# Optimization experiments

Measured on AMD Instinct MI355X. Metric: run time of the kernel, lower is better.

Reference implementation:

```python
import jax, jax.numpy as jnp
import numpy as np

S, B, E = 2048, 2, 768
H = 12
D = E // H  # 64
SCALE = D ** -0.5


def setup_inputs() -> dict:
    key = jax.random.key(0)
    ks = jax.random.split(key, 10)
    inp = {
        "query": jax.random.normal(ks[0], (S, B, E), dtype=jnp.float32),
        "attn_bias": jax.random.normal(ks[1], (B * H, S, S), dtype=jnp.float32) * 0.1,
        "key_padding_mask": jax.random.randint(ks[2], (B, S), 0, 2).astype(bool),
        "Wq": jax.random.normal(ks[3], (E, E), dtype=jnp.float32) * (E ** -0.5),
        "bq": jnp.zeros((E,), dtype=jnp.float32),
        "Wk": jax.random.normal(ks[4], (E, E), dtype=jnp.float32) * (E ** -0.5),
        "bk": jnp.zeros((E,), dtype=jnp.float32),
        "Wv": jax.random.normal(ks[5], (E, E), dtype=jnp.float32) * (E ** -0.5),
        "bv": jnp.zeros((E,), dtype=jnp.float32),
        "Wo": jax.random.normal(ks[6], (E, E), dtype=jnp.float32) * (E ** -0.5),
        "bo": jnp.zeros((E,), dtype=jnp.float32),
    }
    return inp


def reference(query, attn_bias, key_padding_mask, Wq, bq, Wk, bk, Wv, bv, Wo, bo):
    s, b, e = query.shape
    # projections (torch Linear: x @ W.T + b)
    q = (query @ Wq.T + bq) * SCALE
    k = query @ Wk.T + bk
    v = query @ Wv.T + bv
    # [s, b, e] -> [b*h, s, d]
    def to_heads(x):
        return x.reshape(s, b * H, D).transpose(1, 0, 2)
    q, k, v = to_heads(q), to_heads(k), to_heads(v)
    # scores [b*h, s_q, s_k]
    scores = jnp.einsum('nqd,nkd->nqk', q, k) + attn_bias
    # key padding mask: [b, s_k] -> broadcast over heads and queries
    scores = scores.reshape(b, H, s, s)
    scores = jnp.where(key_padding_mask[:, None, None, :], -jnp.inf, scores)
    scores = scores.reshape(b * H, s, s)
    probs = jax.nn.softmax(scores, axis=-1)
    attn = jnp.einsum('nqk,nkd->nqd', probs, v)  # [b*h, s, d]
    attn = attn.transpose(1, 0, 2).reshape(s, b, e)
    return attn @ Wo.T + bo
```

## Files before the change

kernel.cpp:

```cpp
#include <hip/hip_runtime.h>
#include <hip/hip_bf16.h>

typedef __attribute__((ext_vector_type(8))) short s16x8;
typedef __attribute__((ext_vector_type(4))) float f32x4;
typedef unsigned short u16;
typedef unsigned int u32;

#define SDIM 2048
#define BDIM 2
#define HDIM 12
#define DDIM 64
#define EDIM 768
#define MDIM 4096
#define SCALE_Q 0.125f
#define KSPLIT 1024
#define NIT (KSPLIT / 32)
#define HFRAG 131072

static __device__ __forceinline__ f32x4 zero4() {
    f32x4 v; v[0] = v[1] = v[2] = v[3] = 0.f; return v;
}

static __device__ __forceinline__ u16 f2b(float x) {
    u32 u = __builtin_bit_cast(u32, x);
    u32 lsb = (u >> 16) & 1u;
    u += 0x7fffu + lsb;
    return (u16)(u >> 16);
}

static __device__ __forceinline__ f32x4 mfma16(s16x8 a, s16x8 b, f32x4 c) {
    return __builtin_amdgcn_mfma_f32_16x16x32_bf16(a, b, c, 0, 0, 0);
}

static __device__ __forceinline__ void gload_lds16(const void* g, void* l) {
    __builtin_amdgcn_global_load_lds(
        (const __attribute__((address_space(1))) void*)g,
        (__attribute__((address_space(3))) void*)l, 16, 0, 0);
}

__global__ void mask_bits_kernel(const u32* __restrict__ raw, u32* __restrict__ outbits) {
    __shared__ int okInt, okFloat;
    int t = threadIdx.x;
    if (t == 0) { okInt = 1; okFloat = 1; }
    __syncthreads();
    int li = 1, lf = 1;
    for (int i = t; i < 1024; i += blockDim.x) {
        u32 v = raw[i];
        if (v > 1u) li = 0;
        if (v != 0u && v != 0x3F800000u) lf = 0;
    }
    if (!li) atomicAnd(&okInt, 0);
    if (!lf) atomicAnd(&okFloat, 0);
    __syncthreads();
    const unsigned char* rb = (const unsigned char*)raw;
    if (t < (BDIM * SDIM) / 32) {
        u32 bits = 0;
        for (int j = 0; j < 32; ++j) {
            int i = t * 32 + j;
            int v;
            if (okInt)        v = (int)raw[i];
            else if (okFloat) v = (raw[i] != 0u) ? 1 : 0;
            else              v = (int)rb[i];
            bits |= (v ? 1u : 0u) << j;
        }
        outbits[t] = bits;
    }
}

__global__ __launch_bounds__(256) void conv_f32_bf16(
    const float* __restrict__ s, u16* __restrict__ d, int n8)
{
    int i = blockIdx.x * 256 + threadIdx.x;
    if (i >= n8) return;
    float4 x0 = ((const float4*)s)[(size_t)i * 2];
    float4 x1 = ((const float4*)s)[(size_t)i * 2 + 1];
    uint4 o;
    o.x = (u32)f2b(x0.x) | ((u32)f2b(x0.y) << 16);
    o.y = (u32)f2b(x0.z) | ((u32)f2b(x0.w) << 16);
    o.z = (u32)f2b(x1.x) | ((u32)f2b(x1.y) << 16);
    o.w = (u32)f2b(x1.z) | ((u32)f2b(x1.w) << 16);
    ((uint4*)d)[i] = o;
}

__global__ __launch_bounds__(256) void gemm_qkv(
    const u16* __restrict__ A,
    const u16* __restrict__ wq, const u16* __restrict__ wk, const u16* __restrict__ wv,
    const float* __restrict__ bq, const float* __restrict__ bk, const float* __restrict__ bv,
    u16* __restrict__ qout, u16* __restrict__ kout, u16* __restrict__ vout)
{
    __shared__ u16 Al[4096];
    __shared__ u16 Bl[4096];
    int tid = threadIdx.x;
    int lane = tid & 63, w = tid >> 6;
    int r16 = lane & 15, g4 = lane >> 4;
    int wm = w >> 1, wn = w & 1;
    int mb = blockIdx.x * 64;
    int nbg = blockIdx.y * 64;
    int mid = nbg / EDIM;
    int nb = nbg - mid * EDIM;
    const u16* W = (mid == 0) ? wq : (mid == 1) ? wk : wv;
    const float* bias = (mid == 0) ? bq : (mid == 1) ? bk : bv;
    float scale = (mid == 0) ? SCALE_Q : 1.0f;

    f32x4 acc[2][2];
    acc[0][0] = zero4(); acc[0][1] = zero4(); acc[1][0] = zero4(); acc[1][1] = zero4();

    for (int kb = 0; kb < EDIM; kb += 64) {
        __syncthreads();
        #pragma unroll
        for (int j = 0; j < 2; ++j) {
            int c = w * 2 + j;
            gload_lds16(&A[(size_t)(mb + lane) * EDIM + kb + c * 8], (char*)Al + c * 1024);
            gload_lds16(&W[(size_t)(nb + lane) * EDIM + kb + c * 8], (char*)Bl + c * 1024);
        }
        asm volatile("s_waitcnt vmcnt(0)" ::: "memory");
        __syncthreads();
        #pragma unroll
        for (int kk = 0; kk < 2; ++kk) {
            s16x8 a[2], b[2];
            #pragma unroll
            for (int mi = 0; mi < 2; ++mi)
                a[mi] = *(const s16x8*)&Al[(kk * 4 + g4) * 512 + (wm * 32 + mi * 16 + r16) * 8];
            #pragma unroll
            for (int ni = 0; ni < 2; ++ni)
                b[ni] = *(const s16x8*)&Bl[(kk * 4 + g4) * 512 + (wn * 32 + ni * 16 + r16) * 8];
            #pragma unroll
            for (int mi = 0; mi < 2; ++mi)
                #pragma unroll
                for (int ni = 0; ni < 2; ++ni)
                    acc[mi][ni] = mfma16(a[mi], b[ni], acc[mi][ni]);
        }
    }

    #pragma unroll
    for (int mi = 0; mi < 2; ++mi) {
        #pragma unroll
        for (int ni = 0; ni < 2; ++ni) {
            int n = nb + wn * 32 + ni * 16 + r16;
            float bv_ = bias[n];
            #pragma unroll
            for (int r = 0; r < 4; ++r) {
                int m = mb + wm * 32 + mi * 16 + g4 * 4 + r;
                float c = (acc[mi][ni][r] + bv_) * scale;
                int s_ = m >> 1, b_ = m & 1, h_ = n >> 6, d_ = n & 63;
                if (mid == 0) {
                    qout[((size_t)(b_ * HDIM + h_) * SDIM + s_) * DDIM + d_] = f2b(c);
                } else if (mid == 1) {
                    size_t p = (size_t)(b_ * HDIM + h_) * HFRAG
                             + (size_t)(s_ >> 4) * 1024 + (size_t)((d_ >> 5) & 1) * 512
                             + (size_t)(((d_ >> 3) & 3) * 16 + (s_ & 15)) * 8 + (d_ & 7);
                    kout[p] = f2b(c);
                } else {
                    size_t p = (size_t)(b_ * HDIM + h_) * HFRAG
                             + (size_t)(s_ >> 5) * 2048 + (size_t)((d_ >> 4) & 3) * 512
                             + (size_t)(((s_ >> 3) & 3) * 16 + (d_ & 15)) * 8 + (s_ & 7);
                    vout[p] = f2b(c);
                }
            }
        }
    }
}

__global__ __launch_bounds__(256) void gemm_out(
    const u16* __restrict__ A, const u16* __restrict__ Wb,
    const float* __restrict__ bias, float* __restrict__ out_rm)
{
    __shared__ u16 Al[4096];
    __shared__ u16 Bl[4096];
    int tid = threadIdx.x;
    int lane = tid & 63, w = tid >> 6;
    int r16 = lane & 15, g4 = lane >> 4;
    int wm = w >> 1, wn = w & 1;
    int mb = blockIdx.x * 64, nb = blockIdx.y * 64;

    f32x4 acc[2][2];
    acc[0][0] = zero4(); acc[0][1] = zero4(); acc[1][0] = zero4(); acc[1][1] = zero4();

    for (int kb = 0; kb < EDIM; kb += 64) {
        __syncthreads();
        #pragma unroll
        for (int j = 0; j < 2; ++j) {
            int c = w * 2 + j;
            gload_lds16(&A[(size_t)(mb + lane) * EDIM + kb + c * 8], (char*)Al + c * 1024);
            gload_lds16(&Wb[(size_t)(nb + lane) * EDIM + kb + c * 8], (char*)Bl + c * 1024);
        }
        asm volatile("s_waitcnt vmcnt(0)" ::: "memory");
        __syncthreads();
        #pragma unroll
        for (int kk = 0; kk < 2; ++kk) {
            s16x8 a[2], b[2];
            #pragma unroll
            for (int mi = 0; mi < 2; ++mi)
                a[mi] = *(const s16x8*)&Al[(kk * 4 + g4) * 512 + (wm * 32 + mi * 16 + r16) * 8];
            #pragma unroll
            for (int ni = 0; ni < 2; ++ni)
                b[ni] = *(const s16x8*)&Bl[(kk * 4 + g4) * 512 + (wn * 32 + ni * 16 + r16) * 8];
            #pragma unroll
            for (int mi = 0; mi < 2; ++mi)
                #pragma unroll
                for (int ni = 0; ni < 2; ++ni)
                    acc[mi][ni] = mfma16(a[mi], b[ni], acc[mi][ni]);
        }
    }

    #pragma unroll
    for (int mi = 0; mi < 2; ++mi) {
        #pragma unroll
        for (int ni = 0; ni < 2; ++ni) {
            int n = nb + wn * 32 + ni * 16 + r16;
            float bv_ = bias[n];
            #pragma unroll
            for (int r = 0; r < 4; ++r) {
                int m = mb + wm * 32 + mi * 16 + g4 * 4 + r;
                out_rm[(size_t)m * EDIM + n] = acc[mi][ni][r] + bv_;
            }
        }
    }
}

struct KV { s16x8 k0, k1, k2, k3, v0, v1, v2, v3; };

__global__ __launch_bounds__(128) void attn_fused(
    const u16* __restrict__ qw, const u16* __restrict__ kf_g,
    const u16* __restrict__ vf_g, const float* __restrict__ bias,
    const u32* __restrict__ maskBits, u16* __restrict__ attn_out)
{
    __shared__ __align__(1024) unsigned char SM[21504];

    int flat = blockIdx.y * 64 + blockIdx.x;
    int virt = (flat & 7) * 192 + (flat >> 3);
    int qt = virt & 63, bh = virt >> 6;

    int tid = threadIdx.x;
    int w = tid >> 6, lane = tid & 63;
    int r16 = lane & 15, g4 = lane >> 4;
    int qbase = qt * 32;
    int b_ = bh / HDIM, h_ = bh % HDIM;
    const u16* Q  = qw   + (size_t)bh * SDIM * DDIM;
    const u16* KF = kf_g + (size_t)bh * HFRAG;
    const u16* VF = vf_g + (size_t)bh * HFRAG;
    const float* BrowQ = bias + (size_t)bh * SDIM * SDIM + (size_t)qbase * SDIM;
    const u32* mB = maskBits + b_ * (SDIM / 32);

    unsigned char* wb = SM + w * 10752;
    float* RingW = (float*)wb;
    u16*   Pl    = (u16*)(wb + 8192);

    s16x8 qf[2][2];
    #pragma unroll
    for (int h = 0; h < 2; ++h) {
        qf[h][0] = *(const s16x8*)&Q[(size_t)(qbase + 16 * h + r16) * DDIM + g4 * 8];
        qf[h][1] = *(const s16x8*)&Q[(size_t)(qbase + 16 * h + r16) * DDIM + g4 * 8 + 32];
    }

    f32x4 accO[2][4];
    #pragma unroll
    for (int h = 0; h < 2; ++h)
        #pragma unroll
        for (int dt = 0; dt < 4; ++dt) accO[h][dt] = zero4();
    float m_run[2] = {-1e30f, -1e30f}, l_run[2] = {0.f, 0.f};

    const int k0 = w * KSPLIT;

    auto issue_kv = [&](int t, KV& dst) {
        int tc = t < NIT ? t : NIT - 1;
        int kbn = k0 + tc * 32;
        const u16* KT = KF + (size_t)(kbn >> 4) * 1024;
        dst.k0 = *(const s16x8*)&KT[lane * 8];
        dst.k1 = *(const s16x8*)&KT[512 + lane * 8];
        dst.k2 = *(const s16x8*)&KT[1024 + lane * 8];
        dst.k3 = *(const s16x8*)&KT[1536 + lane * 8];
        const u16* VT = VF + (size_t)(kbn >> 5) * 2048;
        dst.v0 = *(const s16x8*)&VT[lane * 8];
        dst.v1 = *(const s16x8*)&VT[512 + lane * 8];
        dst.v2 = *(const s16x8*)&VT[1024 + lane * 8];
        dst.v3 = *(const s16x8*)&VT[1536 + lane * 8];
    };

    auto stage_bias = [&](int t) {
        int tc = t < NIT ? t : NIT - 1;
        int kb = k0 + tc * 32;
        unsigned char* slot = (unsigned char*)(RingW + (t & 1) * 1024);
        int sq = (lane & 7) ^ ((lane >> 3) & 7);
        #pragma unroll
        for (int j = 0; j < 4; ++j) {
            int row = j * 8 + (lane >> 3);
            gload_lds16(&BrowQ[(size_t)row * SDIM + kb + sq * 4], slot + j * 1024);
        }
    };

    auto compute = [&](int t, KV& cur) {
        u32 mw = mB[__builtin_amdgcn_readfirstlane((k0 + t * 32) >> 5)];
        const float* Bs = RingW + (t & 1) * 1024;
        f32x4 sc[2][2];
        __builtin_amdgcn_s_setprio(1);
        #pragma unroll
        for (int h = 0; h < 2; ++h) {
            sc[h][0] = mfma16(cur.k1, qf[h][1], mfma16(cur.k0, qf[h][0], zero4()));
            sc[h][1] = mfma16(cur.k3, qf[h][1], mfma16(cur.k2, qf[h][0], zero4()));
        }
        __builtin_amdgcn_s_setprio(0);
        #pragma unroll
        for (int h = 0; h < 2; ++h) {
            int rr = 16 * h + r16;
            #pragma unroll
            for (int kt = 0; kt < 2; ++kt) {
                float4 bc = *(const float4*)&Bs[rr * 32 + (((4 * kt + g4) ^ (r16 & 7)) * 4)];
                u32 mseg = (mw >> (16 * kt + 4 * g4)) & 0xF;
                sc[h][kt][0] = (mseg & 1) ? -1e30f : sc[h][kt][0] + bc.x;
                sc[h][kt][1] = (mseg & 2) ? -1e30f : sc[h][kt][1] + bc.y;
                sc[h][kt][2] = (mseg & 4) ? -1e30f : sc[h][kt][2] + bc.z;
                sc[h][kt][3] = (mseg & 8) ? -1e30f : sc[h][kt][3] + bc.w;
            }
        }
        #pragma unroll
        for (int h = 0; h < 2; ++h) {
            float pm = fmaxf(
                fmaxf(fmaxf(sc[h][0][0], sc[h][0][1]), fmaxf(sc[h][0][2], sc[h][0][3])),
                fmaxf(fmaxf(sc[h][1][0], sc[h][1][1]), fmaxf(sc[h][1][2], sc[h][1][3])));
            pm = fmaxf(pm, __shfl_xor(pm, 16));
            pm = fmaxf(pm, __shfl_xor(pm, 32));
            bool norescale = __all(pm <= m_run[h] + 4.f);
            float mn = norescale ? m_run[h] : fmaxf(m_run[h], pm);
            float p[8];
            #pragma unroll
            for (int kt = 0; kt < 2; ++kt)
                #pragma unroll
                for (int r = 0; r < 4; ++r)
                    p[kt * 4 + r] = __expf(sc[h][kt][r] - mn);
            float ps = ((p[0] + p[1]) + (p[2] + p[3])) + ((p[4] + p[5]) + (p[6] + p[7]));
            ps += __shfl_xor(ps, 16);
            ps += __shfl_xor(ps, 32);
            if (norescale) {
                l_run[h] += ps;
            } else {
                float alpha = __expf(m_run[h] - mn);
                l_run[h] = l_run[h] * alpha + ps;
                m_run[h] = mn;
                float aR0 = __shfl(alpha, g4 * 4 + 0);
                float aR1 = __shfl(alpha, g4 * 4 + 1);
                float aR2 = __shfl(alpha, g4 * 4 + 2);
                float aR3 = __shfl(alpha, g4 * 4 + 3);
                #pragma unroll
                for (int dt = 0; dt < 4; ++dt) {
                    accO[h][dt][0] *= aR0;
                    accO[h][dt][1] *= aR1;
                    accO[h][dt][2] *= aR2;
                    accO[h][dt][3] *= aR3;
                }
            }
            int rr = 16 * h + r16;
            #pragma unroll
            for (int kt = 0; kt < 2; ++kt) {
                uint2 pv;
                pv.x = (u32)f2b(p[kt * 4 + 0]) | ((u32)f2b(p[kt * 4 + 1]) << 16);
                pv.y = (u32)f2b(p[kt * 4 + 2]) | ((u32)f2b(p[kt * 4 + 3]) << 16);
                *(uint2*)&Pl[rr * 40 + kt * 16 + g4 * 4] = pv;
            }
        }
        __builtin_amdgcn_s_setprio(1);
        #pragma unroll
        for (int h = 0; h < 2; ++h) {
            s16x8 pf = *(const s16x8*)&Pl[(16 * h + r16) * 40 + g4 * 8];
            accO[h][0] = mfma16(pf, cur.v0, accO[h][0]);
            accO[h][1] = mfma16(pf, cur.v1, accO[h][1]);
            accO[h][2] = mfma16(pf, cur.v2, accO[h][2]);
            accO[h][3] = mfma16(pf, cur.v3, accO[h][3]);
        }
        __builtin_amdgcn_s_setprio(0);
    };

    KV A, B;
    issue_kv(0, A);
    stage_bias(0);

    for (int t = 0; t < NIT; t += 2) {
        issue_kv(t + 1, B);
        stage_bias(t + 1);
        asm volatile("s_waitcnt vmcnt(12)" ::: "memory");
        __builtin_amdgcn_sched_barrier(0);
        compute(t, A);

        issue_kv(t + 2, A);
        stage_bias(t + 2);
        asm volatile("s_waitcnt vmcnt(12)" ::: "memory");
        __builtin_amdgcn_sched_barrier(0);
        compute(t + 1, B);
    }

    __syncthreads();
    float* As = (float*)SM;
    float* Ml = (float*)(SM + 17408);
    float* Ll = Ml + 64;
    #pragma unroll
    for (int h = 0; h < 2; ++h)
        #pragma unroll
        for (int dt = 0; dt < 4; ++dt)
            #pragma unroll
            for (int r = 0; r < 4; ++r)
                As[(size_t)(w * 32 + 16 * h + g4 * 4 + r) * 68 + dt * 16 + r16] = accO[h][dt][r];
    if (g4 == 0) {
        #pragma unroll
        for (int h = 0; h < 2; ++h) {
            Ml[w * 32 + 16 * h + r16] = m_run[h];
            Ll[w * 32 + 16 * h + r16] = l_run[h];
        }
    }
    __syncthreads();

    #pragma unroll
    for (int h = 0; h < 2; ++h) {
        #pragma unroll
        for (int dg = 0; dg < 2; ++dg) {
            int d = w * 32 + dg * 16 + r16;
            #pragma unroll
            for (int r = 0; r < 4; ++r) {
                int q = 16 * h + g4 * 4 + r;
                float m0 = Ml[q], m1 = Ml[32 + q];
                float mt = fmaxf(m0, m1);
                float e0 = __expf(m0 - mt), e1 = __expf(m1 - mt);
                float lt = Ll[q] * e0 + Ll[32 + q] * e1;
                float o = (As[(size_t)q * 68 + d] * e0 + As[(size_t)(32 + q) * 68 + d] * e1) / lt;
                attn_out[((size_t)(qbase + q) * BDIM + b_) * EDIM + h_ * DDIM + d] = f2b(o);
            }
        }
    }
}

extern "C" void kernel_launch(void* const* d_in, const int* in_sizes, int n_in,
                              void* d_out, int out_size, void* d_ws, size_t ws_size,
                              hipStream_t stream) {
    const float* query     = (const float*)d_in[0];
    const float* attn_bias = (const float*)d_in[1];
    const u32*   mask_raw  = (const u32*)d_in[2];
    const float* Wq = (const float*)d_in[3];
    const float* bq = (const float*)d_in[4];
    const float* Wk = (const float*)d_in[5];
    const float* bk = (const float*)d_in[6];
    const float* Wv = (const float*)d_in[7];
    const float* bv = (const float*)d_in[8];
    const float* Wo = (const float*)d_in[9];
    const float* bo = (const float*)d_in[10];
    float* out = (float*)d_out;

    char* ws = (char*)d_ws;
    u32* maskB = (u32*)ws;
    const size_t HEADSZ = (size_t)BDIM * HDIM * SDIM * DDIM;
    const size_t WSZ = (size_t)EDIM * EDIM;
    u16* qws = (u16*)(ws + 16384);
    u16* kws = qws + HEADSZ;
    u16* vws = kws + HEADSZ;
    u16* aws = vws + HEADSZ;
    u16* qbf = aws;
    u16* wWq = aws + HEADSZ;
    u16* wWk = wWq + WSZ;
    u16* wWv = wWk + WSZ;
    u16* wWo = wWv + WSZ;

    mask_bits_kernel<<<1, 256, 0, stream>>>(mask_raw, maskB);

    conv_f32_bf16<<<(int)(MDIM * EDIM / 8 / 256), 256, 0, stream>>>(query, qbf, MDIM * EDIM / 8);
    conv_f32_bf16<<<(int)(WSZ / 8 / 256), 256, 0, stream>>>(Wq, wWq, (int)(WSZ / 8));
    conv_f32_bf16<<<(int)(WSZ / 8 / 256), 256, 0, stream>>>(Wk, wWk, (int)(WSZ / 8));
    conv_f32_bf16<<<(int)(WSZ / 8 / 256), 256, 0, stream>>>(Wv, wWv, (int)(WSZ / 8));
    conv_f32_bf16<<<(int)(WSZ / 8 / 256), 256, 0, stream>>>(Wo, wWo, (int)(WSZ / 8));

    dim3 gq(MDIM / 64, (3 * EDIM) / 64);
    gemm_qkv<<<gq, 256, 0, stream>>>(qbf, wWq, wWk, wWv, bq, bk, bv, qws, kws, vws);

    dim3 ga(64, BDIM * HDIM);
    attn_fused<<<ga, 128, 0, stream>>>(qws, kws, vws, attn_bias, maskB, aws);

    dim3 go(MDIM / 64, EDIM / 64);
    gemm_out<<<go, 256, 0, stream>>>(aws, wWo, bo, out);
}
```

Measured before the change: 247.4 us.

## Rework GEMM tile loading, prefetch mask words, use packed bf16 conversion

The QKV and output GEMMs drop async global-to-LDS loads with 64-wide K steps. They now use plain vector loads into a padded 56-stride LDS tile with 32-wide K steps, which doubles the number of barrier-separated iterations. In attention, the key padding mask word is prefetched with the K/V fragments (the wait count is raised to match). The s_setprio hints are removed and the manual bf16 rounding is replaced by the hardware packed convert instruction. Together these touch GEMM staging, attention prefetch, instruction cost and wave scheduling.

```diff
diff --git a/kernel.cpp b/kernel.cpp
--- a/kernel.cpp
+++ b/kernel.cpp
@@ -26,6 +26,12 @@
     u32 lsb = (u >> 16) & 1u;
     u += 0x7fffu + lsb;
     return (u16)(u >> 16);
+}
+
+static __device__ __forceinline__ u32 cvt_pk_bf16(float lo, float hi) {
+    u32 r;
+    asm("v_cvt_pk_bf16_f32 %0, %1, %2" : "=v"(r) : "v"(lo), "v"(hi));
+    return r;
 }
 
 static __device__ __forceinline__ f32x4 mfma16(s16x8 a, s16x8 b, f32x4 c) {
@@ -88,8 +94,8 @@
     const float* __restrict__ bq, const float* __restrict__ bk, const float* __restrict__ bv,
     u16* __restrict__ qout, u16* __restrict__ kout, u16* __restrict__ vout)
 {
-    __shared__ u16 Al[4096];
-    __shared__ u16 Bl[4096];
+    __shared__ u16 Al[64 * 56];
+    __shared__ u16 Bl[64 * 56];
     int tid = threadIdx.x;
     int lane = tid & 63, w = tid >> 6;
     int r16 = lane & 15, g4 = lane >> 4;
@@ -105,31 +111,27 @@
     f32x4 acc[2][2];
     acc[0][0] = zero4(); acc[0][1] = zero4(); acc[1][0] = zero4(); acc[1][1] = zero4();
 
-    for (int kb = 0; kb < EDIM; kb += 64) {
+    int srow = tid >> 2, scol = (tid & 3) * 8;
+
+    for (int kb = 0; kb < EDIM; kb += 32) {
         __syncthreads();
-        #pragma unroll
-        for (int j = 0; j < 2; ++j) {
-            int c = w * 2 + j;
-            gload_lds16(&A[(size_t)(mb + lane) * EDIM + kb + c * 8], (char*)Al + c * 1024);
-            gload_lds16(&W[(size_t)(nb + lane) * EDIM + kb + c * 8], (char*)Bl + c * 1024);
-        }
-        asm volatile("s_waitcnt vmcnt(0)" ::: "memory");
+        *(uint4*)&Al[srow * 56 + scol] =
+            *(const uint4*)&A[(size_t)(mb + srow) * EDIM + kb + scol];
+        *(uint4*)&Bl[srow * 56 + scol] =
+            *(const uint4*)&W[(size_t)(nb + srow) * EDIM + kb + scol];
         __syncthreads();
-        #pragma unroll
-        for (int kk = 0; kk < 2; ++kk) {
-            s16x8 a[2], b[2];
-            #pragma unroll
-            for (int mi = 0; mi < 2; ++mi)
-                a[mi] = *(const s16x8*)&Al[(kk * 4 + g4) * 512 + (wm * 32 + mi * 16 + r16) * 8];
+        s16x8 a[2], bb[2];
+        #pragma unroll
+        for (int mi = 0; mi < 2; ++mi)
+            a[mi] = *(const s16x8*)&Al[(wm * 32 + mi * 16 + r16) * 56 + g4 * 8];
+        #pragma unroll
+        for (int ni = 0; ni < 2; ++ni)
+            bb[ni] = *(const s16x8*)&Bl[(wn * 32 + ni * 16 + r16) * 56 + g4 * 8];
+        #pragma unroll
+        for (int mi = 0; mi < 2; ++mi)
             #pragma unroll
             for (int ni = 0; ni < 2; ++ni)
-                b[ni] = *(const s16x8*)&Bl[(kk * 4 + g4) * 512 + (wn * 32 + ni * 16 + r16) * 8];
-            #pragma unroll
-            for (int mi = 0; mi < 2; ++mi)
-                #pragma unroll
-                for (int ni = 0; ni < 2; ++ni)
-                    acc[mi][ni] = mfma16(a[mi], b[ni], acc[mi][ni]);
-        }
+                acc[mi][ni] = mfma16(a[mi], bb[ni], acc[mi][ni]);
     }
 
     #pragma unroll
@@ -165,8 +167,8 @@
     const u16* __restrict__ A, const u16* __restrict__ Wb,
     const float* __restrict__ bias, float* __restrict__ out_rm)
 {
-    __shared__ u16 Al[4096];
-    __shared__ u16 Bl[4096];
+    __shared__ u16 Al[64 * 56];
+    __shared__ u16 Bl[64 * 56];
     int tid = threadIdx.x;
     int lane = tid & 63, w = tid >> 6;
     int r16 = lane & 15, g4 = lane >> 4;
@@ -176,31 +178,27 @@
     f32x4 acc[2][2];
     acc[0][0] = zero4(); acc[0][1] = zero4(); acc[1][0] = zero4(); acc[1][1] = zero4();
 
-    for (int kb = 0; kb < EDIM; kb += 64) {
+    int srow = tid >> 2, scol = (tid & 3) * 8;
+
+    for (int kb = 0; kb < EDIM; kb += 32) {
         __syncthreads();
-        #pragma unroll
-        for (int j = 0; j < 2; ++j) {
-            int c = w * 2 + j;
-            gload_lds16(&A[(size_t)(mb + lane) * EDIM + kb + c * 8], (char*)Al + c * 1024);
-            gload_lds16(&Wb[(size_t)(nb + lane) * EDIM + kb + c * 8], (char*)Bl + c * 1024);
-        }
-        asm volatile("s_waitcnt vmcnt(0)" ::: "memory");
+        *(uint4*)&Al[srow * 56 + scol] =
+            *(const uint4*)&A[(size_t)(mb + srow) * EDIM + kb + scol];
+        *(uint4*)&Bl[srow * 56 + scol] =
+            *(const uint4*)&Wb[(size_t)(nb + srow) * EDIM + kb + scol];
         __syncthreads();
-        #pragma unroll
-        for (int kk = 0; kk < 2; ++kk) {
-            s16x8 a[2], b[2];
-            #pragma unroll
-            for (int mi = 0; mi < 2; ++mi)
-                a[mi] = *(const s16x8*)&Al[(kk * 4 + g4) * 512 + (wm * 32 + mi * 16 + r16) * 8];
+        s16x8 a[2], bb[2];
+        #pragma unroll
+        for (int mi = 0; mi < 2; ++mi)
+            a[mi] = *(const s16x8*)&Al[(wm * 32 + mi * 16 + r16) * 56 + g4 * 8];
+        #pragma unroll
+        for (int ni = 0; ni < 2; ++ni)
+            bb[ni] = *(const s16x8*)&Bl[(wn * 32 + ni * 16 + r16) * 56 + g4 * 8];
+        #pragma unroll
+        for (int mi = 0; mi < 2; ++mi)
             #pragma unroll
             for (int ni = 0; ni < 2; ++ni)
-                b[ni] = *(const s16x8*)&Bl[(kk * 4 + g4) * 512 + (wn * 32 + ni * 16 + r16) * 8];
-            #pragma unroll
-            for (int mi = 0; mi < 2; ++mi)
-                #pragma unroll
-                for (int ni = 0; ni < 2; ++ni)
-                    acc[mi][ni] = mfma16(a[mi], b[ni], acc[mi][ni]);
-        }
+                acc[mi][ni] = mfma16(a[mi], bb[ni], acc[mi][ni]);
     }
 
     #pragma unroll
@@ -218,7 +216,7 @@
     }
 }
 
-struct KV { s16x8 k0, k1, k2, k3, v0, v1, v2, v3; };
+struct KV { s16x8 k0, k1, k2, k3, v0, v1, v2, v3; u32 mw; };
 
 __global__ __launch_bounds__(128) void attn_fused(
     const u16* __restrict__ qw, const u16* __restrict__ kf_g,
@@ -275,6 +273,7 @@
         dst.v1 = *(const s16x8*)&VT[512 + lane * 8];
         dst.v2 = *(const s16x8*)&VT[1024 + lane * 8];
         dst.v3 = *(const s16x8*)&VT[1536 + lane * 8];
+        dst.mw = mB[kbn >> 5];
     };
 
     auto stage_bias = [&](int t) {
@@ -290,16 +289,14 @@
     };
 
     auto compute = [&](int t, KV& cur) {
-        u32 mw = mB[__builtin_amdgcn_readfirstlane((k0 + t * 32) >> 5)];
+        u32 mw = cur.mw;
         const float* Bs = RingW + (t & 1) * 1024;
         f32x4 sc[2][2];
-        __builtin_amdgcn_s_setprio(1);
         #pragma unroll
         for (int h = 0; h < 2; ++h) {
             sc[h][0] = mfma16(cur.k1, qf[h][1], mfma16(cur.k0, qf[h][0], zero4()));
             sc[h][1] = mfma16(cur.k3, qf[h][1], mfma16(cur.k2, qf[h][0], zero4()));
         }
-        __builtin_amdgcn_s_setprio(0);
         #pragma unroll
         for (int h = 0; h < 2; ++h) {
             int rr = 16 * h + r16;
@@ -353,12 +350,11 @@
             #pragma unroll
             for (int kt = 0; kt < 2; ++kt) {
                 uint2 pv;
-                pv.x = (u32)f2b(p[kt * 4 + 0]) | ((u32)f2b(p[kt * 4 + 1]) << 16);
-                pv.y = (u32)f2b(p[kt * 4 + 2]) | ((u32)f2b(p[kt * 4 + 3]) << 16);
+                pv.x = cvt_pk_bf16(p[kt * 4 + 0], p[kt * 4 + 1]);
+                pv.y = cvt_pk_bf16(p[kt * 4 + 2], p[kt * 4 + 3]);
                 *(uint2*)&Pl[rr * 40 + kt * 16 + g4 * 4] = pv;
             }
         }
-        __builtin_amdgcn_s_setprio(1);
         #pragma unroll
         for (int h = 0; h < 2; ++h) {
             s16x8 pf = *(const s16x8*)&Pl[(16 * h + r16) * 40 + g4 * 8];
@@ -367,7 +363,6 @@
             accO[h][2] = mfma16(pf, cur.v2, accO[h][2]);
             accO[h][3] = mfma16(pf, cur.v3, accO[h][3]);
         }
-        __builtin_amdgcn_s_setprio(0);
     };
 
     KV A, B;
@@ -377,13 +372,13 @@
     for (int t = 0; t < NIT; t += 2) {
         issue_kv(t + 1, B);
         stage_bias(t + 1);
-        asm volatile("s_waitcnt vmcnt(12)" ::: "memory");
+        asm volatile("s_waitcnt vmcnt(13)" ::: "memory");
         __builtin_amdgcn_sched_barrier(0);
         compute(t, A);
 
         issue_kv(t + 2, A);
         stage_bias(t + 2);
-        asm volatile("s_waitcnt vmcnt(12)" ::: "memory");
+        asm volatile("s_waitcnt vmcnt(13)" ::: "memory");
         __builtin_amdgcn_sched_barrier(0);
         compute(t + 1, B);
     }
```

Result: faster. 228.6 us (-7.6%).
